# Optimization experiments

Hardware: AMD Instinct MI355X
Metric: run time of the kernel (lower is better)

## Reference

```python
import jax, jax.numpy as jnp
import numpy as np

N, D, F = 10000, 16, 256  # nodes, uniform degree, feature dim (F_in == F_out required by module)


def setup_inputs() -> dict:
    key = jax.random.key(0)
    ks = jax.random.split(key, 8)
    s = 0.05  # small param scale (xavier-like) to keep exp() in a sane range
    return {
        "nodes": jax.random.normal(ks[0], (N, F), jnp.float32),
        "neighbors": jax.random.normal(ks[1], (N, D, F), jnp.float32),
        "aspects": jax.random.normal(ks[2], (N, D, F), jnp.float32),
        "Wp": jax.random.normal(ks[3], (F, F), jnp.float32) * s,      # linear_proj.weight
        "Wa": jax.random.normal(ks[4], (F, 2 * F), jnp.float32) * s,  # aspect_linear_proj.weight
        "ba": jnp.zeros((F,), jnp.float32),                           # aspect_linear_proj.bias
        "a_src": jax.random.normal(ks[5], (F,), jnp.float32) * s,     # scoring_fn_source
        "a_tgt": jax.random.normal(ks[6], (F,), jnp.float32) * s,     # scoring_fn_target
        "bias": jnp.zeros((F,), jnp.float32),                         # output bias
    }


def reference(nodes, neighbors, aspects, Wp, Wa, ba, a_src, a_tgt, bias):
    # target scores from projected node features: [N]
    nodes_proj = nodes @ Wp.T                                   # [N, F]
    scores_target = (nodes_proj * a_tgt).sum(-1)                # [N]

    # project neighbors and aspects with the shared linear_proj: [N, D, F]
    n_proj = jnp.einsum('ndf,gf->ndg', neighbors, Wp)
    a_proj = jnp.einsum('ndf,gf->ndg', aspects, Wp)

    # linear aspects method: concat projected features, then aspect Linear
    na = jnp.concatenate([n_proj, a_proj], axis=-1)             # [N, D, 2F]
    na_proj = jnp.einsum('ndk,fk->ndf', na, Wa) + ba            # [N, D, F]

    scores_source = (na_proj * a_src).sum(-1)                   # [N, D]
    scores = jax.nn.leaky_relu(scores_source + scores_target[:, None], 0.2)

    # module uses raw exp / (sum + 1e-16), not max-subtracted softmax
    e = jnp.exp(scores)                                         # [N, D]
    attn = e / (e.sum(axis=1, keepdims=True) + 1e-16)

    out = jnp.einsum('ndf,nd->nf', n_proj, attn)                # [N, F]
    return jax.nn.elu(out + bias)
```

## Files before the change

kernel.cpp:

```cpp
#include <hip/hip_runtime.h>
#include <hip/hip_bf16.h>
#include <math.h>

#define NN 10000
#define DD 16
#define FF 256

typedef float f32x4 __attribute__((ext_vector_type(4)));

#define DOT4(a, b) ((a)[0]*(b)[0] + (a)[1]*(b)[1] + (a)[2]*(b)[2] + (a)[3]*(b)[3])


__global__ __launch_bounds__(256) void k_pre1(
    const float* __restrict__ Wp, const float* __restrict__ Wa,
    const float* __restrict__ a_src, const float* __restrict__ a_tgt,
    float* __restrict__ part) {
  const int t = threadIdx.x, b = blockIdx.x;
  float s1 = 0.f, s2 = 0.f, vt = 0.f;
  #pragma unroll
  for (int k = 0; k < 16; ++k) {
    const int f = b * 16 + k;
    const float as = a_src[f];
    s1 += as * Wa[f * 2 * FF + t];
    s2 += as * Wa[f * 2 * FF + FF + t];
    vt += a_tgt[f] * Wp[f * FF + t];
  }
  part[(b * 3 + 0) * FF + t] = s1;
  part[(b * 3 + 1) * FF + t] = s2;
  part[(b * 3 + 2) * FF + t] = vt;
}

__global__ __launch_bounds__(256) void k_pre2(
    const float* __restrict__ Wp, const float* __restrict__ ba,
    const float* __restrict__ a_src, const float* __restrict__ part,
    float* __restrict__ pre) {
  __shared__ float w1[FF], w2[FF];
  __shared__ float pu1[8][32], pu2[8][32];
  const int t = threadIdx.x;

  float a0 = 0.f, a1 = 0.f, a2 = 0.f;
  #pragma unroll
  for (int b = 0; b < 16; ++b) {
    a0 += part[(b * 3 + 0) * FF + t];
    a1 += part[(b * 3 + 1) * FF + t];
    a2 += part[(b * 3 + 2) * FF + t];
  }
  w1[t] = a0; w2[t] = a1;
  if (blockIdx.x == 0) {
    pre[t] = a2;
    if (t < 64) {
      float cp = 0.f;
      #pragma unroll
      for (int k = 0; k < 4; ++k) cp += ba[t + 64 * k] * a_src[t + 64 * k];
      #pragma unroll
      for (int o = 32; o > 0; o >>= 1) cp += __shfl_xor(cp, o);
      if (t == 0) pre[3 * FF] = cp;
    }
  }
  __syncthreads();

  const int tc = t & 31;
  const int gc = t >> 5;
  const int tt = blockIdx.x * 32 + tc;
  float u1 = 0.f, u2 = 0.f;
  #pragma unroll 4
  for (int g = gc * 32; g < gc * 32 + 32; ++g) {
    const float wpg = Wp[g * FF + tt];
    u1 += w1[g] * wpg;
    u2 += w2[g] * wpg;
  }
  pu1[gc][tc] = u1; pu2[gc][tc] = u2;
  __syncthreads();
  if (t < 32) {
    float r1 = 0.f, r2 = 0.f;
    #pragma unroll
    for (int k = 0; k < 8; ++k) { r1 += pu1[k][t]; r2 += pu2[k][t]; }
    pre[FF + blockIdx.x * 32 + t] = r1;
    pre[2 * FF + blockIdx.x * 32 + t] = r2;
  }
}

__global__ __launch_bounds__(256) void k_attn_agg(
    const float* __restrict__ nodes, const float* __restrict__ neighbors,
    const float* __restrict__ aspects, const float* __restrict__ pre,
    float* __restrict__ agg) {
  const int lane = threadIdx.x & 63;
  const int n = (blockIdx.x << 2) + (threadIdx.x >> 6);

  const f32x4 vtv = ((const f32x4*)(pre))[lane];
  const f32x4 u1v = ((const f32x4*)(pre + FF))[lane];
  const f32x4 u2v = ((const f32x4*)(pre + 2 * FF))[lane];
  const float c0 = pre[3 * FF];

  const f32x4* __restrict__ nbg = (const f32x4*)(neighbors + (size_t)n * DD * FF);
  const f32x4* __restrict__ asg = (const f32x4*)(aspects + (size_t)n * DD * FF);

  f32x4 nbv[DD], asv[DD];
  #pragma unroll
  for (int r = 0; r < DD; ++r) nbv[r] = __builtin_nontemporal_load(&nbg[r * 64 + lane]);
  #pragma unroll
  for (int r = 0; r < DD; ++r) asv[r] = __builtin_nontemporal_load(&asg[r * 64 + lane]);
  const f32x4 nv = ((const f32x4*)(nodes + (size_t)n * FF))[lane];

  float p[DD + 1];
  #pragma unroll
  for (int r = 0; r < DD; ++r)
    p[r] = DOT4(nbv[r], u1v) + DOT4(asv[r], u2v);
  p[DD] = DOT4(nv, vtv);

  #pragma unroll
  for (int o = 32; o > 0; o >>= 1) {
    #pragma unroll
    for (int r = 0; r < DD + 1; ++r) p[r] += __shfl_xor(p[r], o);
  }

  float e[DD], esum = 0.f;
  #pragma unroll
  for (int r = 0; r < DD; ++r) {
    float s = p[r] + p[DD] + c0;
    s = s > 0.f ? s : 0.2f * s;
    e[r] = __expf(s);
    esum += e[r];
  }
  const float inv = 1.f / (esum + 1e-16f);

  f32x4 acc = (f32x4)(0.f);
  #pragma unroll
  for (int r = 0; r < DD; ++r) {
    acc[0] += e[r] * nbv[r][0];
    acc[1] += e[r] * nbv[r][1];
    acc[2] += e[r] * nbv[r][2];
    acc[3] += e[r] * nbv[r][3];
  }
  acc[0] *= inv; acc[1] *= inv; acc[2] *= inv; acc[3] *= inv;
  ((f32x4*)(agg + (size_t)n * FF))[lane] = acc;
}

#define TN 16
__global__ __launch_bounds__(256) void k_proj_out(
    const float* __restrict__ Wp, const float* __restrict__ bias,
    float* __restrict__ out) {
  const int t = threadIdx.x;
  const int n0 = blockIdx.x * TN;
  __shared__ float ag[TN][FF];

  #pragma unroll
  for (int i = 0; i < TN; ++i)
    ag[i][t] = out[(size_t)(n0 + i) * FF + t];
  __syncthreads();

  float acc[TN];
  #pragma unroll
  for (int i = 0; i < TN; ++i) acc[i] = 0.f;

  const float4* wrow = (const float4*)(Wp + (size_t)t * FF);
  for (int f4 = 0; f4 < FF / 4; ++f4) {
    float4 w = wrow[f4];
    #pragma unroll
    for (int i = 0; i < TN; ++i) {
      float4 a = ((const float4*)&ag[i][0])[f4];
      acc[i] += a.x * w.x + a.y * w.y + a.z * w.z + a.w * w.w;
    }
  }

  const float b = bias[t];
  #pragma unroll
  for (int i = 0; i < TN; ++i) {
    float v = acc[i] + b;
    out[(size_t)(n0 + i) * FF + t] = v > 0.f ? v : expm1f(v);
  }
}

extern "C" void kernel_launch(void* const* d_in, const int* in_sizes, int n_in,
                              void* d_out, int out_size, void* d_ws, size_t ws_size,
                              hipStream_t stream) {
  const float* nodes     = (const float*)d_in[0];
  const float* neighbors = (const float*)d_in[1];
  const float* aspects   = (const float*)d_in[2];
  const float* Wp        = (const float*)d_in[3];
  const float* Wa        = (const float*)d_in[4];
  const float* ba        = (const float*)d_in[5];
  const float* a_src     = (const float*)d_in[6];
  const float* a_tgt     = (const float*)d_in[7];
  const float* bias      = (const float*)d_in[8];
  float* out = (float*)d_out;
  float* pre = (float*)d_ws;

  float* part = out + (size_t)NN * FF - 16 * 3 * FF;

  k_pre1<<<16, 256, 0, stream>>>(Wp, Wa, a_src, a_tgt, part);
  k_pre2<<<8, 256, 0, stream>>>(Wp, ba, a_src, part, pre);
  k_attn_agg<<<NN / 4, 256, 0, stream>>>(nodes, neighbors, aspects, pre, out);
  k_proj_out<<<NN / TN, 256, 0, stream>>>(Wp, bias, out);
}
```

Before: 119.1 us.

## Split each node's attention across a full block with shared-memory neighbor staging

Instead of one wavefront per node holding all 16 neighbor and aspect rows in registers, each node now gets a 256-thread block. Each wavefront loads 4 rows, computes partial scores, writes them to shared memory, and after a barrier every thread aggregates one feature column from neighbors staged in LDS. The aim is to cut register pressure and raise memory-level parallelism for this bandwidth-bound phase. The cost is a block barrier, 16KB of LDS per block and redundant node/vt dot products in every wave.

After: 116.0 us. -2.5%, faster.

```diff
diff --git a/kernel.cpp b/kernel.cpp
--- a/kernel.cpp
+++ b/kernel.cpp
@@ -7,7 +7,6 @@
 #define FF 256
 
 typedef float f32x4 __attribute__((ext_vector_type(4)));
-
 #define DOT4(a, b) ((a)[0]*(b)[0] + (a)[1]*(b)[1] + (a)[2]*(b)[2] + (a)[3]*(b)[3])
 
 
@@ -84,56 +83,72 @@
     const float* __restrict__ nodes, const float* __restrict__ neighbors,
     const float* __restrict__ aspects, const float* __restrict__ pre,
     float* __restrict__ agg) {
-  const int lane = threadIdx.x & 63;
-  const int n = (blockIdx.x << 2) + (threadIdx.x >> 6);
-
-  const f32x4 vtv = ((const f32x4*)(pre))[lane];
+  const int n = blockIdx.x;
+  const int tid = threadIdx.x;
+  const int wid = tid >> 6;
+  const int lane = tid & 63;
+
+  __shared__ float nb[DD][FF];
+  __shared__ float sc[DD];
+
+  const f32x4* nbg = (const f32x4*)(neighbors + (size_t)n * DD * FF);
+  const f32x4* asg = (const f32x4*)(aspects + (size_t)n * DD * FF);
+  const f32x4* ndp = (const f32x4*)(nodes + (size_t)n * FF);
+
+  f32x4 nbv[4], asv[4];
+  #pragma unroll
+  for (int k = 0; k < 4; ++k)
+    nbv[k] = __builtin_nontemporal_load(&nbg[(wid + 4 * k) * (FF / 4) + lane]);
+  #pragma unroll
+  for (int k = 0; k < 4; ++k)
+    asv[k] = __builtin_nontemporal_load(&asg[(wid + 4 * k) * (FF / 4) + lane]);
+  f32x4 nv = ndp[lane];
+
   const f32x4 u1v = ((const f32x4*)(pre + FF))[lane];
   const f32x4 u2v = ((const f32x4*)(pre + 2 * FF))[lane];
+  const f32x4 vtv = ((const f32x4*)(pre))[lane];
   const float c0 = pre[3 * FF];
 
-  const f32x4* __restrict__ nbg = (const f32x4*)(neighbors + (size_t)n * DD * FF);
-  const f32x4* __restrict__ asg = (const f32x4*)(aspects + (size_t)n * DD * FF);
-
-  f32x4 nbv[DD], asv[DD];
-  #pragma unroll
-  for (int r = 0; r < DD; ++r) nbv[r] = __builtin_nontemporal_load(&nbg[r * 64 + lane]);
-  #pragma unroll
-  for (int r = 0; r < DD; ++r) asv[r] = __builtin_nontemporal_load(&asg[r * 64 + lane]);
-  const f32x4 nv = ((const f32x4*)(nodes + (size_t)n * FF))[lane];
-
-  float p[DD + 1];
-  #pragma unroll
-  for (int r = 0; r < DD; ++r)
-    p[r] = DOT4(nbv[r], u1v) + DOT4(asv[r], u2v);
-  p[DD] = DOT4(nv, vtv);
+  #pragma unroll
+  for (int k = 0; k < 4; ++k)
+    ((f32x4*)&nb[wid + 4 * k][0])[lane] = nbv[k];
+
+  float p[4];
+  #pragma unroll
+  for (int k = 0; k < 4; ++k)
+    p[k] = DOT4(nbv[k], u1v) + DOT4(asv[k], u2v);
+  float st = DOT4(nv, vtv);
 
   #pragma unroll
   for (int o = 32; o > 0; o >>= 1) {
+    p[0] += __shfl_xor(p[0], o);
+    p[1] += __shfl_xor(p[1], o);
+    p[2] += __shfl_xor(p[2], o);
+    p[3] += __shfl_xor(p[3], o);
+    st   += __shfl_xor(st, o);
+  }
+  if (lane == 0) {
     #pragma unroll
-    for (int r = 0; r < DD + 1; ++r) p[r] += __shfl_xor(p[r], o);
-  }
-
-  float e[DD], esum = 0.f;
-  #pragma unroll
-  for (int r = 0; r < DD; ++r) {
-    float s = p[r] + p[DD] + c0;
+    for (int k = 0; k < 4; ++k) sc[wid + 4 * k] = p[k] + st + c0;
+  }
+  __syncthreads();
+
+  float e[DD];
+  float esum = 0.f;
+  #pragma unroll
+  for (int d = 0; d < DD; ++d) {
+    float s = sc[d];
     s = s > 0.f ? s : 0.2f * s;
-    e[r] = __expf(s);
-    esum += e[r];
+    float ev = __expf(s);
+    e[d] = ev;
+    esum += ev;
   }
   const float inv = 1.f / (esum + 1e-16f);
 
-  f32x4 acc = (f32x4)(0.f);
-  #pragma unroll
-  for (int r = 0; r < DD; ++r) {
-    acc[0] += e[r] * nbv[r][0];
-    acc[1] += e[r] * nbv[r][1];
-    acc[2] += e[r] * nbv[r][2];
-    acc[3] += e[r] * nbv[r][3];
-  }
-  acc[0] *= inv; acc[1] *= inv; acc[2] *= inv; acc[3] *= inv;
-  ((f32x4*)(agg + (size_t)n * FF))[lane] = acc;
+  float acc = 0.f;
+  #pragma unroll
+  for (int d = 0; d < DD; ++d) acc += e[d] * nb[d][tid];
+  agg[(size_t)n * FF + tid] = acc * inv;
 }
 
 #define TN 16
@@ -190,6 +205,6 @@
 
   k_pre1<<<16, 256, 0, stream>>>(Wp, Wa, a_src, a_tgt, part);
   k_pre2<<<8, 256, 0, stream>>>(Wp, ba, a_src, part, pre);
-  k_attn_agg<<<NN / 4, 256, 0, stream>>>(nodes, neighbors, aspects, pre, out);
+  k_attn_agg<<<NN, 256, 0, stream>>>(nodes, neighbors, aspects, pre, out);
   k_proj_out<<<NN / TN, 256, 0, stream>>>(Wp, bias, out);
 }
```

## Fuse attention aggregation with output projection into one kernel via shared memory

Applied to the files above, without the earlier changes.

Merges the attention/aggregation kernel and the output projection kernel into one launch. Each block now handles 16 nodes, with each wave looping over 4 nodes and writing the aggregated vector to shared memory, which the projection then reads directly. This removes the global round trip of the intermediate and one kernel launch. The grid shrinks from 2500 to 625 blocks, and aspect loads are now consumed as they stream in rather than held in registers, which cuts memory parallelism per wave and may hurt latency hiding on a bandwidth-bound load.

Measured after the change: 113.0 us. 1.05x faster.

```diff
diff --git a/kernel.cpp b/kernel.cpp
--- a/kernel.cpp
+++ b/kernel.cpp
@@ -5,9 +5,9 @@
 #define NN 10000
 #define DD 16
 #define FF 256
+#define TN 16
 
 typedef float f32x4 __attribute__((ext_vector_type(4)));
-
 #define DOT4(a, b) ((a)[0]*(b)[0] + (a)[1]*(b)[1] + (a)[2]*(b)[2] + (a)[3]*(b)[3])
 
 
@@ -80,94 +80,97 @@
   }
 }
 
-__global__ __launch_bounds__(256) void k_attn_agg(
+__global__ __launch_bounds__(256) void k_fused(
     const float* __restrict__ nodes, const float* __restrict__ neighbors,
     const float* __restrict__ aspects, const float* __restrict__ pre,
-    float* __restrict__ agg) {
-  const int lane = threadIdx.x & 63;
-  const int n = (blockIdx.x << 2) + (threadIdx.x >> 6);
+    const float* __restrict__ Wp, const float* __restrict__ bias,
+    float* __restrict__ out) {
+  const int tid = threadIdx.x;
+  const int wid = tid >> 6;
+  const int lane = tid & 63;
+  const int n0 = blockIdx.x * TN;
 
-  const f32x4 vtv = ((const f32x4*)(pre))[lane];
+  __shared__ float ag[TN][FF];
+
   const f32x4 u1v = ((const f32x4*)(pre + FF))[lane];
   const f32x4 u2v = ((const f32x4*)(pre + 2 * FF))[lane];
+  const f32x4 vtv = ((const f32x4*)(pre))[lane];
   const float c0 = pre[3 * FF];
 
-  const f32x4* __restrict__ nbg = (const f32x4*)(neighbors + (size_t)n * DD * FF);
-  const f32x4* __restrict__ asg = (const f32x4*)(aspects + (size_t)n * DD * FF);
+  #pragma unroll 1
+  for (int j = 0; j < 4; ++j) {
+    const int i = wid * 4 + j;
+    const int n = n0 + i;
+    const f32x4* __restrict__ nbg = (const f32x4*)(neighbors + (size_t)n * DD * FF);
+    const f32x4* __restrict__ asg = (const f32x4*)(aspects + (size_t)n * DD * FF);
 
-  f32x4 nbv[DD], asv[DD];
-  #pragma unroll
-  for (int r = 0; r < DD; ++r) nbv[r] = __builtin_nontemporal_load(&nbg[r * 64 + lane]);
-  #pragma unroll
-  for (int r = 0; r < DD; ++r) asv[r] = __builtin_nontemporal_load(&asg[r * 64 + lane]);
-  const f32x4 nv = ((const f32x4*)(nodes + (size_t)n * FF))[lane];
+    f32x4 nbv[DD];
+    #pragma unroll
+    for (int r = 0; r < DD; ++r)
+      nbv[r] = __builtin_nontemporal_load(&nbg[r * 64 + lane]);
 
-  float p[DD + 1];
-  #pragma unroll
-  for (int r = 0; r < DD; ++r)
-    p[r] = DOT4(nbv[r], u1v) + DOT4(asv[r], u2v);
-  p[DD] = DOT4(nv, vtv);
+    float p[DD + 1];
+    #pragma unroll
+    for (int r = 0; r < DD; ++r) p[r] = DOT4(nbv[r], u1v);
 
-  #pragma unroll
-  for (int o = 32; o > 0; o >>= 1) {
     #pragma unroll
-    for (int r = 0; r < DD + 1; ++r) p[r] += __shfl_xor(p[r], o);
+    for (int r = 0; r < DD; ++r) {
+      const f32x4 av = __builtin_nontemporal_load(&asg[r * 64 + lane]);
+      p[r] += DOT4(av, u2v);
+    }
+    const f32x4 nv = ((const f32x4*)(nodes + (size_t)n * FF))[lane];
+    p[DD] = DOT4(nv, vtv);
+
+    #pragma unroll
+    for (int o = 32; o > 0; o >>= 1) {
+      #pragma unroll
+      for (int r = 0; r < DD + 1; ++r) p[r] += __shfl_xor(p[r], o);
+    }
+
+    float esum = 0.f;
+    float e[DD];
+    #pragma unroll
+    for (int r = 0; r < DD; ++r) {
+      float s = p[r] + p[DD] + c0;
+      s = s > 0.f ? s : 0.2f * s;
+      e[r] = __expf(s);
+      esum += e[r];
+    }
+    const float inv = 1.f / (esum + 1e-16f);
+
+    f32x4 acc = (f32x4)(0.f);
+    #pragma unroll
+    for (int r = 0; r < DD; ++r) {
+      acc[0] += e[r] * nbv[r][0];
+      acc[1] += e[r] * nbv[r][1];
+      acc[2] += e[r] * nbv[r][2];
+      acc[3] += e[r] * nbv[r][3];
+    }
+    acc[0] *= inv; acc[1] *= inv; acc[2] *= inv; acc[3] *= inv;
+    ((f32x4*)&ag[i][0])[lane] = acc;
   }
 
-  float e[DD], esum = 0.f;
-  #pragma unroll
-  for (int r = 0; r < DD; ++r) {
-    float s = p[r] + p[DD] + c0;
-    s = s > 0.f ? s : 0.2f * s;
-    e[r] = __expf(s);
-    esum += e[r];
-  }
-  const float inv = 1.f / (esum + 1e-16f);
-
-  f32x4 acc = (f32x4)(0.f);
-  #pragma unroll
-  for (int r = 0; r < DD; ++r) {
-    acc[0] += e[r] * nbv[r][0];
-    acc[1] += e[r] * nbv[r][1];
-    acc[2] += e[r] * nbv[r][2];
-    acc[3] += e[r] * nbv[r][3];
-  }
-  acc[0] *= inv; acc[1] *= inv; acc[2] *= inv; acc[3] *= inv;
-  ((f32x4*)(agg + (size_t)n * FF))[lane] = acc;
-}
-
-#define TN 16
-__global__ __launch_bounds__(256) void k_proj_out(
-    const float* __restrict__ Wp, const float* __restrict__ bias,
-    float* __restrict__ out) {
-  const int t = threadIdx.x;
-  const int n0 = blockIdx.x * TN;
-  __shared__ float ag[TN][FF];
-
-  #pragma unroll
-  for (int i = 0; i < TN; ++i)
-    ag[i][t] = out[(size_t)(n0 + i) * FF + t];
   __syncthreads();
 
   float acc[TN];
   #pragma unroll
   for (int i = 0; i < TN; ++i) acc[i] = 0.f;
 
-  const float4* wrow = (const float4*)(Wp + (size_t)t * FF);
+  const f32x4* wrow = (const f32x4*)(Wp + (size_t)tid * FF);
   for (int f4 = 0; f4 < FF / 4; ++f4) {
-    float4 w = wrow[f4];
+    const f32x4 w = wrow[f4];
     #pragma unroll
     for (int i = 0; i < TN; ++i) {
-      float4 a = ((const float4*)&ag[i][0])[f4];
-      acc[i] += a.x * w.x + a.y * w.y + a.z * w.z + a.w * w.w;
+      const f32x4 a = ((const f32x4*)&ag[i][0])[f4];
+      acc[i] += DOT4(a, w);
     }
   }
 
-  const float b = bias[t];
+  const float b = bias[tid];
   #pragma unroll
   for (int i = 0; i < TN; ++i) {
     float v = acc[i] + b;
-    out[(size_t)(n0 + i) * FF + t] = v > 0.f ? v : expm1f(v);
+    out[(size_t)(n0 + i) * FF + tid] = v > 0.f ? v : expm1f(v);
   }
 }
 
@@ -190,6 +193,5 @@
 
   k_pre1<<<16, 256, 0, stream>>>(Wp, Wa, a_src, a_tgt, part);
   k_pre2<<<8, 256, 0, stream>>>(Wp, ba, a_src, part, pre);
-  k_attn_agg<<<NN / 4, 256, 0, stream>>>(nodes, neighbors, aspects, pre, out);
-  k_proj_out<<<NN / TN, 256, 0, stream>>>(Wp, bias, out);
+  k_fused<<<NN / TN, 256, 0, stream>>>(nodes, neighbors, aspects, pre, Wp, bias, out);
 }
```
